# Kernel tuning notes

Measured on AMD Instinct MI355X. Metric: run time of the kernel, lower is better.

Reference implementation:

```python
import jax, jax.numpy as jnp
import numpy as np

DIM = 1024
NUM_HEADS = 16
HEAD_DIM = DIM // NUM_HEADS
TGT_LEN = 4096


def setup_inputs() -> dict:
    key = jax.random.key(0)
    k1, k2, k3 = jax.random.split(key, 3)
    x = jax.random.normal(k1, (TGT_LEN, DIM), dtype=jnp.float32)
    W_in = jax.random.normal(k2, (3 * DIM, DIM), dtype=jnp.float32) * (DIM ** -0.5)
    W_out = jax.random.normal(k3, (DIM, DIM), dtype=jnp.float32) * (DIM ** -0.5)
    return {"x": x, "W_in": W_in, "W_out": W_out, "tgt_len": TGT_LEN}


def reference(x, W_in, W_out, tgt_len):
    # QKV projection (torch Linear: y = x @ W^T)
    qkv = x @ W_in.T  # [T, 3*dim]
    q, k, v = jnp.split(qkv, 3, axis=-1)
    # [T, dim] -> [H, T, hd]
    q = q.reshape(tgt_len, NUM_HEADS, HEAD_DIM).transpose(1, 0, 2)
    k = k.reshape(tgt_len, NUM_HEADS, HEAD_DIM).transpose(1, 0, 2)
    v = v.reshape(tgt_len, NUM_HEADS, HEAD_DIM).transpose(1, 0, 2)
    scaling = HEAD_DIM ** -0.5
    scores = jnp.einsum('htd,hsd->hts', q, k) * scaling  # [H, T, T]
    # joint softmax over the full (T, T) matrix per head (NOT row-wise)
    maxes = jnp.max(scores, axis=(1, 2), keepdims=True)
    x_exp = jnp.exp(scores - maxes)
    probs = x_exp / jnp.sum(x_exp, axis=(1, 2), keepdims=True)
    attn = jnp.einsum('hts,hsd->htd', probs, v)  # [H, T, hd]
    attn = attn.transpose(1, 0, 2).reshape(tgt_len, DIM)
    return attn @ W_out.T
```

## Files before the change

### kernel.cpp

```cpp
#include <hip/hip_runtime.h>

#define TLEN 4096
#define DIM 1024
#define NHEAD 16
#define HDIM 64
#define QKV_COLS (3 * DIM)
#define QSCALE 0.1803368801111244f
#define NCHUNK 2
#define SCHUNK (TLEN / NCHUNK)

typedef __attribute__((ext_vector_type(8))) short short8;
typedef __attribute__((ext_vector_type(4))) float f32x4;

struct alignas(8) s4 { short v[4]; };

__device__ float g_Lsum[NHEAD];
__device__ float g_recipL[NHEAD];

__global__ void zeroL() {
    if (threadIdx.x < NHEAD) g_Lsum[threadIdx.x] = 0.0f;
}
__global__ void recipL() {
    if (threadIdx.x < NHEAD) g_recipL[threadIdx.x] = 1.0f / g_Lsum[threadIdx.x];
}

__device__ __forceinline__ unsigned bf16_rtne_bits(float x) {
    unsigned u = __float_as_uint(x);
    return (u + 0x7fffu + ((u >> 16) & 1u)) >> 16;
}

__device__ __forceinline__ void cp16(const short* g, short* l) {
    __builtin_amdgcn_global_load_lds(
        (const __attribute__((address_space(1))) unsigned int*)g,
        (__attribute__((address_space(3))) unsigned int*)l,
        16, 0, 0);
}

__global__ __launch_bounds__(256) void conv_bf16(
    const float* __restrict__ src, short* __restrict__ dst, int n4)
{
    int i = blockIdx.x * 256 + threadIdx.x;
    if (i < n4) {
        float4 v = ((const float4*)src)[i];
        s4 o;
        o.v[0] = (short)bf16_rtne_bits(v.x);
        o.v[1] = (short)bf16_rtne_bits(v.y);
        o.v[2] = (short)bf16_rtne_bits(v.z);
        o.v[3] = (short)bf16_rtne_bits(v.w);
        ((s4*)dst)[i] = o;
    }
}

__global__ __launch_bounds__(256) void conv_wout(
    const float* __restrict__ src, short* __restrict__ dst)
{
    int i = blockIdx.x * 256 + threadIdx.x;
    float s = g_recipL[(i & 255) >> 4];
    float4 v = ((const float4*)src)[i];
    s4 o;
    o.v[0] = (short)bf16_rtne_bits(v.x * s);
    o.v[1] = (short)bf16_rtne_bits(v.y * s);
    o.v[2] = (short)bf16_rtne_bits(v.z * s);
    o.v[3] = (short)bf16_rtne_bits(v.w * s);
    ((s4*)dst)[i] = o;
}

__global__ __launch_bounds__(256) void combine(
    const short* __restrict__ p0, const short* __restrict__ p1,
    short* __restrict__ dst, int n4)
{
    int i = blockIdx.x * 256 + threadIdx.x;
    if (i < n4) {
        s4 a = ((const s4*)p0)[i];
        s4 b = ((const s4*)p1)[i];
        s4 o;
#pragma unroll
        for (int m = 0; m < 4; ++m) {
            float fa = __uint_as_float(((unsigned)(unsigned short)a.v[m]) << 16);
            float fb = __uint_as_float(((unsigned)(unsigned short)b.v[m]) << 16);
            o.v[m] = (short)bf16_rtne_bits(fa + fb);
        }
        ((s4*)dst)[i] = o;
    }
}

template <bool QKV_MODE>
__global__ __launch_bounds__(256) void gemm_bt(
    const short* __restrict__ A, const short* __restrict__ B,
    void* __restrict__ Cout, short* __restrict__ Vout, int M, int N, int K)
{
    __shared__ __align__(16) short As[128][32];
    __shared__ __align__(16) short Bs[128][32];
    const int tid  = threadIdx.x;
    const int wv   = tid >> 6, lane = tid & 63;
    const int fr   = lane & 15, quad = lane >> 4;
    const int wm   = (wv >> 1) * 64, wn = (wv & 1) * 64;
    const int m0 = blockIdx.x * 128, n0 = blockIdx.y * 128;

    f32x4 acc[4][4] = {};

    for (int k0 = 0; k0 < K; k0 += 32) {
        __syncthreads();
#pragma unroll
        for (int c = tid; c < 512; c += 256) {
            int row = c >> 2, col = (c & 3) * 8;
            cp16(A + (size_t)(m0 + row) * K + k0 + col, &As[row][col]);
            cp16(B + (size_t)(n0 + row) * K + k0 + col, &Bs[row][col]);
        }
        __syncthreads();

        short8 af[4], bfr[4];
#pragma unroll
        for (int i = 0; i < 4; ++i) {
            af[i]  = *(const short8*)&As[wm + i * 16 + fr][quad * 8];
            bfr[i] = *(const short8*)&Bs[wn + i * 16 + fr][quad * 8];
        }
#pragma unroll
        for (int i = 0; i < 4; ++i)
#pragma unroll
            for (int j = 0; j < 4; ++j)
                acc[i][j] = __builtin_amdgcn_mfma_f32_16x16x32_bf16(af[i], bfr[j], acc[i][j], 0, 0, 0);
    }

    if (QKV_MODE && n0 >= 2 * DIM) {
#pragma unroll
        for (int i = 0; i < 4; ++i)
#pragma unroll
            for (int j = 0; j < 4; ++j) {
                int n = n0 - 2 * DIM + wn + j * 16 + fr;
                int m = m0 + wm + i * 16 + quad * 4;
                unsigned u0 = bf16_rtne_bits(acc[i][j][0]);
                unsigned u1 = bf16_rtne_bits(acc[i][j][1]);
                unsigned u2 = bf16_rtne_bits(acc[i][j][2]);
                unsigned u3 = bf16_rtne_bits(acc[i][j][3]);
                uint2 pk;
                pk.x = u0 | (u1 << 16);
                pk.y = u2 | (u3 << 16);
                *(uint2*)(Vout + (size_t)n * TLEN + m) = pk;
            }
    } else if (QKV_MODE) {
        const float sc = (n0 < DIM) ? QSCALE : 1.0f;
#pragma unroll
        for (int i = 0; i < 4; ++i)
#pragma unroll
            for (int j = 0; j < 4; ++j)
#pragma unroll
                for (int r = 0; r < 4; ++r) {
                    size_t off = (size_t)(m0 + wm + i * 16 + quad * 4 + r) * N + n0 + wn + j * 16 + fr;
                    ((short*)Cout)[off] = (short)bf16_rtne_bits(acc[i][j][r] * sc);
                }
    } else {
#pragma unroll
        for (int i = 0; i < 4; ++i)
#pragma unroll
            for (int j = 0; j < 4; ++j)
#pragma unroll
                for (int r = 0; r < 4; ++r) {
                    size_t off = (size_t)(m0 + wm + i * 16 + quad * 4 + r) * N + n0 + wn + j * 16 + fr;
                    ((float*)Cout)[off] = acc[i][j][r];
                }
    }
}

__global__ __launch_bounds__(256) void attn_mfma(
    const short* __restrict__ qkvb, const short* __restrict__ vtb,
    short* __restrict__ part)
{
    __shared__ short Ks[64][72];
    __shared__ short Vt[64][72];
    __shared__ short Ps[128][72];
    __shared__ float red[256];

    const int tid = threadIdx.x;
    const int t0 = blockIdx.x * 128;
    const int h  = blockIdx.y;
    const int chunk = blockIdx.z;
    const int srow = tid >> 2;
    const int sch  = (tid & 3) * 16;
    const int wv   = tid >> 6;
    const int lane = tid & 63;
    const int fr   = lane & 15;
    const int quad = lane >> 4;
    const int tb   = wv * 32;

#pragma unroll
    for (int half = 0; half < 128; half += 64) {
        const short* src = qkvb + (size_t)(t0 + half + srow) * QKV_COLS + h * HDIM + sch;
        uint4 a = *(const uint4*)(src);
        uint4 b = *(const uint4*)(src + 8);
        *(uint4*)&Ps[half + srow][sch]     = a;
        *(uint4*)&Ps[half + srow][sch + 8] = b;
    }
    __syncthreads();

    short8 qf[2][2];
#pragma unroll
    for (int jt = 0; jt < 2; ++jt)
#pragma unroll
        for (int kh = 0; kh < 2; ++kh)
            qf[jt][kh] = *(const short8*)&Ps[tb + jt * 16 + fr][kh * 32 + quad * 8];

    short8 ones;
#pragma unroll
    for (int m = 0; m < 8; ++m) ones[m] = (short)0x3F80;

    f32x4 oaccT[4][2] = {};
    f32x4 racc[2] = {};

    for (int s0 = chunk * SCHUNK; s0 < (chunk + 1) * SCHUNK; s0 += 64) {
        __syncthreads();
        {
            const short* ksrc = qkvb + (size_t)(s0 + srow) * QKV_COLS + DIM + h * HDIM + sch;
            uint4 ka = *(const uint4*)(ksrc);
            uint4 kb = *(const uint4*)(ksrc + 8);
            const short* vsrc = vtb + (size_t)(h * HDIM + srow) * TLEN + s0 + sch;
            uint4 va = *(const uint4*)(vsrc);
            uint4 vb = *(const uint4*)(vsrc + 8);
            *(uint4*)&Ks[srow][sch]     = ka;
            *(uint4*)&Ks[srow][sch + 8] = kb;
            *(uint4*)&Vt[srow][sch]     = va;
            *(uint4*)&Vt[srow][sch + 8] = vb;
        }
        __syncthreads();

#pragma unroll
        for (int i = 0; i < 4; ++i) {
            short8 ka0 = *(const short8*)&Ks[i * 16 + fr][quad * 8];
            short8 ka1 = *(const short8*)&Ks[i * 16 + fr][32 + quad * 8];
#pragma unroll
            for (int jt = 0; jt < 2; ++jt) {
                f32x4 acc = {};
                acc = __builtin_amdgcn_mfma_f32_16x16x32_bf16(ka0, qf[jt][0], acc, 0, 0, 0);
                acc = __builtin_amdgcn_mfma_f32_16x16x32_bf16(ka1, qf[jt][1], acc, 0, 0, 0);
                unsigned u0 = __float_as_uint(__builtin_amdgcn_exp2f(acc[0]));
                unsigned u1 = __float_as_uint(__builtin_amdgcn_exp2f(acc[1]));
                unsigned u2 = __float_as_uint(__builtin_amdgcn_exp2f(acc[2]));
                unsigned u3 = __float_as_uint(__builtin_amdgcn_exp2f(acc[3]));
                uint2 pk;
                pk.x = __builtin_amdgcn_perm(u1, u0, 0x07060302);
                pk.y = __builtin_amdgcn_perm(u3, u2, 0x07060302);
                *(uint2*)&Ps[tb + jt * 16 + fr][i * 16 + quad * 4] = pk;
            }
        }

        short8 pb[2][2];
#pragma unroll
        for (int jt = 0; jt < 2; ++jt)
#pragma unroll
            for (int kh = 0; kh < 2; ++kh)
                pb[jt][kh] = *(const short8*)&Ps[tb + jt * 16 + fr][kh * 32 + quad * 8];

#pragma unroll
        for (int jt = 0; jt < 2; ++jt) {
            racc[jt] = __builtin_amdgcn_mfma_f32_16x16x32_bf16(ones, pb[jt][0], racc[jt], 0, 0, 0);
            racc[jt] = __builtin_amdgcn_mfma_f32_16x16x32_bf16(ones, pb[jt][1], racc[jt], 0, 0, 0);
        }
#pragma unroll
        for (int jd = 0; jd < 4; ++jd) {
            short8 va0 = *(const short8*)&Vt[jd * 16 + fr][quad * 8];
            short8 va1 = *(const short8*)&Vt[jd * 16 + fr][32 + quad * 8];
#pragma unroll
            for (int jt = 0; jt < 2; ++jt) {
                oaccT[jd][jt] = __builtin_amdgcn_mfma_f32_16x16x32_bf16(va0, pb[jt][0], oaccT[jd][jt], 0, 0, 0);
                oaccT[jd][jt] = __builtin_amdgcn_mfma_f32_16x16x32_bf16(va1, pb[jt][1], oaccT[jd][jt], 0, 0, 0);
            }
        }
    }

    short* pc = part + (size_t)chunk * TLEN * DIM;
#pragma unroll
    for (int jt = 0; jt < 2; ++jt)
#pragma unroll
        for (int jd = 0; jd < 4; ++jd) {
            unsigned u0 = bf16_rtne_bits(oaccT[jd][jt][0]);
            unsigned u1 = bf16_rtne_bits(oaccT[jd][jt][1]);
            unsigned u2 = bf16_rtne_bits(oaccT[jd][jt][2]);
            unsigned u3 = bf16_rtne_bits(oaccT[jd][jt][3]);
            uint2 pk;
            pk.x = u0 | (u1 << 16);
            pk.y = u2 | (u3 << 16);
            *(uint2*)(pc + (size_t)(t0 + tb + jt * 16 + fr) * DIM + h * HDIM + jd * 16 + quad * 4) = pk;
        }

    red[tid] = (racc[0][0] + racc[1][0]) * 0.25f;
    __syncthreads();
    for (int off = 128; off > 0; off >>= 1) {
        if (tid < off) red[tid] += red[tid + off];
        __syncthreads();
    }
    if (tid == 0) atomicAdd(&g_Lsum[h], red[0]);
}

extern "C" void kernel_launch(void* const* d_in, const int* in_sizes, int n_in,
                              void* d_out, int out_size, void* d_ws, size_t ws_size,
                              hipStream_t stream)
{
    const float* x     = (const float*)d_in[0];
    const float* W_in  = (const float*)d_in[1];
    const float* W_out = (const float*)d_in[2];
    float* out = (float*)d_out;

    char* ws = (char*)d_ws;
    short* xb    = (short*)(ws);
    short* wib   = (short*)(ws + (8u << 20));
    short* wob   = (short*)(ws + (14u << 20));
    short* qkvb  = (short*)(ws + (16u << 20));
    short* vtb   = (short*)(ws + (40u << 20));
    short* part  = (short*)(ws + (48u << 20));
    short* attnb = xb;

    zeroL<<<1, 64, 0, stream>>>();

    conv_bf16<<<(TLEN * DIM / 4 + 255) / 256, 256, 0, stream>>>(x, xb, TLEN * DIM / 4);
    conv_bf16<<<(QKV_COLS * DIM / 4 + 255) / 256, 256, 0, stream>>>(W_in, wib, QKV_COLS * DIM / 4);

    gemm_bt<true><<<dim3(TLEN / 128, QKV_COLS / 128), 256, 0, stream>>>(
        xb, wib, qkvb, vtb, TLEN, QKV_COLS, DIM);

    attn_mfma<<<dim3(TLEN / 128, NHEAD, NCHUNK), 256, 0, stream>>>(qkvb, vtb, part);

    recipL<<<1, 64, 0, stream>>>();
    conv_wout<<<(DIM * DIM / 4 + 255) / 256, 256, 0, stream>>>(W_out, wob);

    combine<<<(TLEN * DIM / 4 + 255) / 256, 256, 0, stream>>>(
        part, part + (size_t)TLEN * DIM, attnb, TLEN * DIM / 4);

    gemm_bt<false><<<dim3(TLEN / 128, DIM / 128), 256, 0, stream>>>(
        attnb, wob, out, nullptr, TLEN, DIM, DIM);
}
```

Measured before the change: 254.4 us.

## Keep P in registers via permlane swaps, double query tile, prefetch K/V

The attention kernel now gives each wave 64 query rows, so a block covers 256, which doubles reuse of every K/V tile loaded into LDS. The exponentiated score fragments are rearranged into the MFMA B-operand layout with permlane32/permlane16 swaps instead of a round trip through a shared P buffer. The next K/V tile is prefetched into registers while the current one is being computed. In exchange, register pressure goes up (launch bounds now ask for 2 blocks per CU) and the grid has half as many blocks.

```diff
diff --git a/kernel.cpp b/kernel.cpp
--- a/kernel.cpp
+++ b/kernel.cpp
@@ -8,6 +8,7 @@
 #define QSCALE 0.1803368801111244f
 #define NCHUNK 2
 #define SCHUNK (TLEN / NCHUNK)
+#define TB 256
 
 typedef __attribute__((ext_vector_type(8))) short short8;
 typedef __attribute__((ext_vector_type(4))) float f32x4;
@@ -34,6 +35,12 @@
         (const __attribute__((address_space(1))) unsigned int*)g,
         (__attribute__((address_space(3))) unsigned int*)l,
         16, 0, 0);
+}
+
+__device__ __forceinline__ short8 mk8(unsigned a, unsigned b, unsigned c, unsigned d) {
+    union { unsigned u[4]; short8 s; } t;
+    t.u[0] = a; t.u[1] = b; t.u[2] = c; t.u[3] = d;
+    return t.s;
 }
 
 __global__ __launch_bounds__(256) void conv_bf16(
@@ -162,17 +169,16 @@
     }
 }
 
-__global__ __launch_bounds__(256) void attn_mfma(
+__global__ __launch_bounds__(256, 2) void attn_mfma(
     const short* __restrict__ qkvb, const short* __restrict__ vtb,
     short* __restrict__ part)
 {
-    __shared__ short Ks[64][72];
-    __shared__ short Vt[64][72];
-    __shared__ short Ps[128][72];
+    __shared__ __align__(16) short Ks[64][72];
+    __shared__ __align__(16) short Vt[64][72];
     __shared__ float red[256];
 
     const int tid = threadIdx.x;
-    const int t0 = blockIdx.x * 128;
+    const int t0 = blockIdx.x * TB;
     const int h  = blockIdx.y;
     const int chunk = blockIdx.z;
     const int srow = tid >> 2;
@@ -181,95 +187,100 @@
     const int lane = tid & 63;
     const int fr   = lane & 15;
     const int quad = lane >> 4;
-    const int tb   = wv * 32;
-
-#pragma unroll
-    for (int half = 0; half < 128; half += 64) {
-        const short* src = qkvb + (size_t)(t0 + half + srow) * QKV_COLS + h * HDIM + sch;
-        uint4 a = *(const uint4*)(src);
-        uint4 b = *(const uint4*)(src + 8);
-        *(uint4*)&Ps[half + srow][sch]     = a;
-        *(uint4*)&Ps[half + srow][sch + 8] = b;
-    }
-    __syncthreads();
-
-    short8 qf[2][2];
-#pragma unroll
-    for (int jt = 0; jt < 2; ++jt)
-#pragma unroll
-        for (int kh = 0; kh < 2; ++kh)
-            qf[jt][kh] = *(const short8*)&Ps[tb + jt * 16 + fr][kh * 32 + quad * 8];
+    const int tb   = wv * 64;
+
+    short8 qf[4][2];
+#pragma unroll
+    for (int jt = 0; jt < 4; ++jt) {
+        const short* qsrc = qkvb + (size_t)(t0 + tb + jt * 16 + fr) * QKV_COLS + h * HDIM + quad * 8;
+        qf[jt][0] = *(const short8*)qsrc;
+        qf[jt][1] = *(const short8*)(qsrc + 32);
+    }
 
     short8 ones;
 #pragma unroll
     for (int m = 0; m < 8; ++m) ones[m] = (short)0x3F80;
 
-    f32x4 oaccT[4][2] = {};
-    f32x4 racc[2] = {};
-
-    for (int s0 = chunk * SCHUNK; s0 < (chunk + 1) * SCHUNK; s0 += 64) {
-        __syncthreads();
-        {
-            const short* ksrc = qkvb + (size_t)(s0 + srow) * QKV_COLS + DIM + h * HDIM + sch;
-            uint4 ka = *(const uint4*)(ksrc);
-            uint4 kb = *(const uint4*)(ksrc + 8);
-            const short* vsrc = vtb + (size_t)(h * HDIM + srow) * TLEN + s0 + sch;
-            uint4 va = *(const uint4*)(vsrc);
-            uint4 vb = *(const uint4*)(vsrc + 8);
-            *(uint4*)&Ks[srow][sch]     = ka;
-            *(uint4*)&Ks[srow][sch + 8] = kb;
-            *(uint4*)&Vt[srow][sch]     = va;
-            *(uint4*)&Vt[srow][sch + 8] = vb;
-        }
-        __syncthreads();
-
+    f32x4 oaccT[4][4] = {};
+    f32x4 racc[4] = {};
+
+    const int s_begin = chunk * SCHUNK;
+    const short* kbase = qkvb + DIM + h * HDIM + sch;
+    const short* vbase = vtb + (size_t)(h * HDIM + srow) * TLEN + sch;
+
+    uint4 kA, kB, vA, vB;
+    {
+        const short* ks = kbase + (size_t)(s_begin + srow) * QKV_COLS;
+        kA = *(const uint4*)ks;  kB = *(const uint4*)(ks + 8);
+        const short* vs = vbase + s_begin;
+        vA = *(const uint4*)vs;  vB = *(const uint4*)(vs + 8);
+    }
+
+    for (int it = 0; it < SCHUNK / 64; ++it) {
+        *(uint4*)&Ks[srow][sch]     = kA;
+        *(uint4*)&Ks[srow][sch + 8] = kB;
+        *(uint4*)&Vt[srow][sch]     = vA;
+        *(uint4*)&Vt[srow][sch + 8] = vB;
+        __syncthreads();
+
+        if (it + 1 < SCHUNK / 64) {
+            const int s0n = s_begin + (it + 1) * 64;
+            const short* ks = kbase + (size_t)(s0n + srow) * QKV_COLS;
+            kA = *(const uint4*)ks;  kB = *(const uint4*)(ks + 8);
+            const short* vs = vbase + s0n;
+            vA = *(const uint4*)vs;  vB = *(const uint4*)(vs + 8);
+        }
+
+        short8 kf[4][2], vf[4][2];
 #pragma unroll
         for (int i = 0; i < 4; ++i) {
-            short8 ka0 = *(const short8*)&Ks[i * 16 + fr][quad * 8];
-            short8 ka1 = *(const short8*)&Ks[i * 16 + fr][32 + quad * 8];
-#pragma unroll
-            for (int jt = 0; jt < 2; ++jt) {
+            kf[i][0] = *(const short8*)&Ks[i * 16 + fr][quad * 8];
+            kf[i][1] = *(const short8*)&Ks[i * 16 + fr][32 + quad * 8];
+            vf[i][0] = *(const short8*)&Vt[i * 16 + fr][quad * 8];
+            vf[i][1] = *(const short8*)&Vt[i * 16 + fr][32 + quad * 8];
+        }
+
+#pragma unroll
+        for (int jt = 0; jt < 4; ++jt) {
+            unsigned w0[4], w1[4];
+#pragma unroll
+            for (int i = 0; i < 4; ++i) {
                 f32x4 acc = {};
-                acc = __builtin_amdgcn_mfma_f32_16x16x32_bf16(ka0, qf[jt][0], acc, 0, 0, 0);
-                acc = __builtin_amdgcn_mfma_f32_16x16x32_bf16(ka1, qf[jt][1], acc, 0, 0, 0);
+                acc = __builtin_amdgcn_mfma_f32_16x16x32_bf16(kf[i][0], qf[jt][0], acc, 0, 0, 0);
+                acc = __builtin_amdgcn_mfma_f32_16x16x32_bf16(kf[i][1], qf[jt][1], acc, 0, 0, 0);
                 unsigned u0 = __float_as_uint(__builtin_amdgcn_exp2f(acc[0]));
                 unsigned u1 = __float_as_uint(__builtin_amdgcn_exp2f(acc[1]));
                 unsigned u2 = __float_as_uint(__builtin_amdgcn_exp2f(acc[2]));
                 unsigned u3 = __float_as_uint(__builtin_amdgcn_exp2f(acc[3]));
-                uint2 pk;
-                pk.x = __builtin_amdgcn_perm(u1, u0, 0x07060302);
-                pk.y = __builtin_amdgcn_perm(u3, u2, 0x07060302);
-                *(uint2*)&Ps[tb + jt * 16 + fr][i * 16 + quad * 4] = pk;
+                w0[i] = __builtin_amdgcn_perm(u1, u0, 0x07060302);
+                w1[i] = __builtin_amdgcn_perm(u3, u2, 0x07060302);
             }
-        }
-
-        short8 pb[2][2];
-#pragma unroll
-        for (int jt = 0; jt < 2; ++jt)
-#pragma unroll
-            for (int kh = 0; kh < 2; ++kh)
-                pb[jt][kh] = *(const short8*)&Ps[tb + jt * 16 + fr][kh * 32 + quad * 8];
-
-#pragma unroll
-        for (int jt = 0; jt < 2; ++jt) {
-            racc[jt] = __builtin_amdgcn_mfma_f32_16x16x32_bf16(ones, pb[jt][0], racc[jt], 0, 0, 0);
-            racc[jt] = __builtin_amdgcn_mfma_f32_16x16x32_bf16(ones, pb[jt][1], racc[jt], 0, 0, 0);
-        }
-#pragma unroll
-        for (int jd = 0; jd < 4; ++jd) {
-            short8 va0 = *(const short8*)&Vt[jd * 16 + fr][quad * 8];
-            short8 va1 = *(const short8*)&Vt[jd * 16 + fr][32 + quad * 8];
-#pragma unroll
-            for (int jt = 0; jt < 2; ++jt) {
-                oaccT[jd][jt] = __builtin_amdgcn_mfma_f32_16x16x32_bf16(va0, pb[jt][0], oaccT[jd][jt], 0, 0, 0);
-                oaccT[jd][jt] = __builtin_amdgcn_mfma_f32_16x16x32_bf16(va1, pb[jt][1], oaccT[jd][jt], 0, 0, 0);
+            auto A0 = __builtin_amdgcn_permlane32_swap(w0[0], w0[1], false, false);
+            auto A2 = __builtin_amdgcn_permlane32_swap(w0[2], w0[3], false, false);
+            auto B0 = __builtin_amdgcn_permlane32_swap(w1[0], w1[1], false, false);
+            auto B2 = __builtin_amdgcn_permlane32_swap(w1[2], w1[3], false, false);
+            auto O0 = __builtin_amdgcn_permlane16_swap(A0[0], A0[1], false, false);
+            auto O2 = __builtin_amdgcn_permlane16_swap(A2[0], A2[1], false, false);
+            auto P0 = __builtin_amdgcn_permlane16_swap(B0[0], B0[1], false, false);
+            auto P2 = __builtin_amdgcn_permlane16_swap(B2[0], B2[1], false, false);
+            short8 pb0 = mk8(O0[0], P0[0], O0[1], P0[1]);
+            short8 pb1 = mk8(O2[0], P2[0], O2[1], P2[1]);
+
+            racc[jt] = __builtin_amdgcn_mfma_f32_16x16x32_bf16(ones, pb0, racc[jt], 0, 0, 0);
+            racc[jt] = __builtin_amdgcn_mfma_f32_16x16x32_bf16(ones, pb1, racc[jt], 0, 0, 0);
+
+#pragma unroll
+            for (int jd = 0; jd < 4; ++jd) {
+                oaccT[jd][jt] = __builtin_amdgcn_mfma_f32_16x16x32_bf16(vf[jd][0], pb0, oaccT[jd][jt], 0, 0, 0);
+                oaccT[jd][jt] = __builtin_amdgcn_mfma_f32_16x16x32_bf16(vf[jd][1], pb1, oaccT[jd][jt], 0, 0, 0);
             }
         }
+        __syncthreads();
     }
 
     short* pc = part + (size_t)chunk * TLEN * DIM;
 #pragma unroll
-    for (int jt = 0; jt < 2; ++jt)
+    for (int jt = 0; jt < 4; ++jt)
 #pragma unroll
         for (int jd = 0; jd < 4; ++jd) {
             unsigned u0 = bf16_rtne_bits(oaccT[jd][jt][0]);
@@ -282,7 +293,7 @@
             *(uint2*)(pc + (size_t)(t0 + tb + jt * 16 + fr) * DIM + h * HDIM + jd * 16 + quad * 4) = pk;
         }
 
-    red[tid] = (racc[0][0] + racc[1][0]) * 0.25f;
+    red[tid] = (racc[0][0] + racc[1][0] + racc[2][0] + racc[3][0]) * 0.25f;
     __syncthreads();
     for (int off = 128; off > 0; off >>= 1) {
         if (tid < off) red[tid] += red[tid + off];
@@ -317,7 +328,7 @@
     gemm_bt<true><<<dim3(TLEN / 128, QKV_COLS / 128), 256, 0, stream>>>(
         xb, wib, qkvb, vtb, TLEN, QKV_COLS, DIM);
 
-    attn_mfma<<<dim3(TLEN / 128, NHEAD, NCHUNK), 256, 0, stream>>>(qkvb, vtb, part);
+    attn_mfma<<<dim3(TLEN / TB, NHEAD, NCHUNK), 256, 0, stream>>>(qkvb, vtb, part);
 
     recipL<<<1, 64, 0, stream>>>();
     conv_wout<<<(DIM * DIM / 4 + 255) / 256, 256, 0, stream>>>(W_out, wob);
```

After: 220.4 us. 1.15x faster.
